# Kernel optimization log

Hardware: AMD Instinct MI355X
Metric: run time of the kernel (lower is better)

## Reference

```python
import jax, jax.numpy as jnp
import numpy as np

STRIDE = 16      # image -> feature stride (224 -> 14)
POOL = 7         # ROI pool output grid
FG_HI = 0.85
FG_LO = 0.5


def setup_inputs() -> dict:
    key = jax.random.key(0)
    ks = jax.random.split(key, 8)
    B, N, M, K = 4, 128, 16, 80
    Cf, Tf, Cs, Ts, H, W = 256, 32, 2048, 8, 14, 14
    fast = jax.random.normal(ks[0], (B, Cf, Tf, H, W), jnp.float32)
    slow = jax.random.normal(ks[1], (B, Cs, Ts, H, W), jnp.float32)
    # valid gt boxes inside 224x224
    xy = jax.random.uniform(ks[2], (B, M, 2)) * 160.0
    wh = 32.0 + jax.random.uniform(ks[3], (B, M, 2)) * 48.0
    gt = jnp.concatenate([xy, xy + wh], axis=-1)
    # proposals: first M coincide with gt (guarantees IoU>=0.85 foreground), rest random
    pxy = jax.random.uniform(ks[4], (B, N - M, 2)) * 160.0
    pwh = 16.0 + jax.random.uniform(ks[5], (B, N - M, 2)) * 64.0
    props = jnp.concatenate([gt, jnp.concatenate([pxy, pxy + pwh], axis=-1)], axis=1)
    gt_classes = (jax.random.uniform(ks[6], (B, M, K)) < 0.1).astype(jnp.float32)
    C = Cf + Cs
    W_cls = jax.random.normal(ks[7], (C, K), jnp.float32) * 0.02
    b_cls = jnp.zeros((K,), jnp.float32)
    return dict(fast_feature=fast, slow_feature=slow, proposal_bboxes=props,
                gt_bboxes_batch=gt, gt_classes_batch=gt_classes,
                W_cls=W_cls, b_cls=b_cls)


def _iou(a, b):
    # a: [B,N,4], b: [B,M,4] (x1,y1,x2,y2) -> [B,N,M]
    tl = jnp.maximum(a[:, :, None, :2], b[:, None, :, :2])
    br = jnp.minimum(a[:, :, None, 2:], b[:, None, :, 2:])
    inter = jnp.prod(jnp.clip(br - tl, 0.0), axis=-1)
    area_a = jnp.prod(a[:, :, 2:] - a[:, :, :2], axis=-1)[:, :, None]
    area_b = jnp.prod(b[:, :, 2:] - b[:, :, :2], axis=-1)[:, None, :]
    return inter / (area_a + area_b - inter)


def _roi_pool(feat, boxes):
    # feat: [B,C,H,W]; boxes: [B,N,4] in image coords -> [B,N,P,P,C]
    B, C, H, W = feat.shape
    fb = boxes / STRIDE
    x1, y1, x2, y2 = fb[..., 0], fb[..., 1], fb[..., 2], fb[..., 3]
    grid = (jnp.arange(POOL, dtype=feat.dtype) + 0.5) / POOL          # [P]
    cy = y1[..., None] + grid * (y2 - y1)[..., None]                  # [B,N,P]
    cx = x1[..., None] + grid * (x2 - x1)[..., None]                  # [B,N,P]
    iy = jnp.clip(jnp.floor(cy), 0, H - 1).astype(jnp.int32)
    ix = jnp.clip(jnp.floor(cx), 0, W - 1).astype(jnp.int32)
    ft = jnp.transpose(feat, (0, 2, 3, 1))                            # [B,H,W,C]
    bidx = jnp.arange(B)[:, None, None, None]
    return ft[bidx, iy[:, :, :, None], ix[:, :, None, :]]             # [B,N,P,P,C]


def reference(fast_feature, slow_feature, proposal_bboxes, gt_bboxes_batch,
              gt_classes_batch, W_cls, b_cls):
    # temporal average pooling (AvgPool3d over full T) + channel concat, fast first
    fast = fast_feature.mean(axis=2)
    slow = slow_feature.mean(axis=2)
    feature = jnp.concatenate([fast, slow], axis=1)                   # [B,C,H,W]

    # IoU-based foreground assignment
    ious = _iou(proposal_bboxes, gt_bboxes_batch)                     # [B,N,M]
    max_ious = ious.max(axis=2)                                       # [B,N]
    assign = ious.argmax(axis=2)                                      # [B,N]
    fg_hi = max_ious >= FG_HI
    fg = jnp.where(fg_hi.any(), fg_hi, max_ious >= FG_LO)             # global fallback
    labels = jnp.take_along_axis(gt_classes_batch, assign[:, :, None], axis=1)  # [B,N,K]

    # ROI pooling (dense over all proposals; non-fg are masked out of the loss)
    pool = _roi_pool(feature, proposal_bboxes)                        # [B,N,P,P,C]
    hid = pool.mean(axis=(2, 3))                                      # [B,N,C]
    logits = jnp.einsum('bnc,ck->bnk', hid, W_cls) + b_cls            # [B,N,K]

    # multilabel soft margin loss per proposal (mean over classes)
    per = -(labels * jax.nn.log_sigmoid(logits)
            + (1.0 - labels) * jax.nn.log_sigmoid(-logits)).mean(axis=-1)  # [B,N]
    fgf = fg.astype(per.dtype)
    cnt = fgf.sum(axis=1)
    cross_entropies = jnp.where(cnt > 0, (per * fgf).sum(axis=1) / jnp.maximum(cnt, 1.0), 0.0)
    return cross_entropies  # [B]
```

## Files before the change

kernel.cpp:

```cpp
#include <hip/hip_runtime.h>
#include <math.h>

#define BB 4
#define NN 128
#define MM 16
#define KK 80
#define CF 256
#define CSL 2048
#define CT 2304
#define TFAST 32
#define TSLOW 8
#define HH 14
#define WW 14
#define HWQ 196
#define NQ4 49

#define G_OFF      0
#define G_SIZE     (BB*HWQ*KK)
#define FGF_OFF    (G_OFF + G_SIZE)
#define ASSIGN_OFF (FGF_OFF + BB*NN)
#define NUM_OFF    (ASSIGN_OFF + BB*NN)
#define CNT_OFF    (NUM_OFF + BB)
#define CTR_OFF    (CNT_OFF + BB)
#define P_OFF      (CTR_OFF + 8)

#define NSPLIT 64
#define MAXCH  43
#define P_SIZE (NSPLIT*G_SIZE)

__global__ __launch_bounds__(256) void k12_fused(const float* __restrict__ fastp,
                                                 const float* __restrict__ slowp,
                                                 const float* __restrict__ Wc,
                                                 float* __restrict__ ws,
                                                 int use_partials) {
    __shared__ float sfeat[MAXCH*HWQ + 64];
    __shared__ float sW[MAXCH*KK];
    int bid = blockIdx.x;
    int b = bid >> 6;
    int r = bid & 63;
    int gc0, nch, T, isfast;
    if (r < 16) { isfast = 1; gc0 = r * 16; nch = 16; T = TFAST; }
    else {
        int s = r - 16;
        int c0s = (s < 32) ? (43 * s) : (1376 + 42 * (s - 32));
        nch = (s < 32) ? 43 : 42;
        gc0 = CF + c0s; T = TSLOW; isfast = 0;
    }
    int tid = threadIdx.x;

    const float4* base = isfast
        ? ((const float4*)fastp + (size_t)(b * CF + gc0) * TFAST * NQ4)
        : ((const float4*)slowp + (size_t)(b * CSL + (gc0 - CF)) * TSLOW * NQ4);
    const float scale = 1.f / (float)T;
    int ntasks = nch * NQ4;
    for (int x = tid; x < ntasks; x += 256) {
        int cl = x / NQ4;
        int q  = x - cl * NQ4;
        const float4* p = base + (size_t)cl * T * NQ4 + q;
        float4 a = make_float4(0.f, 0.f, 0.f, 0.f);
        #pragma unroll 8
        for (int t = 0; t < T; ++t) {
            float4 v = p[t * NQ4];
            a.x += v.x; a.y += v.y; a.z += v.z; a.w += v.w;
        }
        a.x *= scale; a.y *= scale; a.z *= scale; a.w *= scale;
        ((float4*)sfeat)[cl * NQ4 + q] = a;
    }
    const float4* wsrc = (const float4*)Wc + (size_t)gc0 * (KK / 4);
    int wtasks = nch * (KK / 4);
    for (int x = tid; x < wtasks; x += 256) ((float4*)sW)[x] = wsrc[x];
    __syncthreads();

    int cg = tid & 31;
    int kq = tid >> 5;
    float acc[7][10];
    #pragma unroll
    for (int j = 0; j < 7; ++j)
        #pragma unroll
        for (int i = 0; i < 10; ++i) acc[j][i] = 0.f;

    const float* fr = sfeat + cg;
    const float* wr = sW + kq * 10;
    for (int c = 0; c < nch; ++c) {
        float w[10];
        #pragma unroll
        for (int i = 0; i < 10; ++i) w[i] = wr[c * KK + i];
        #pragma unroll
        for (int j = 0; j < 7; ++j) {
            float fv = fr[c * HWQ + 32 * j];
            #pragma unroll
            for (int i = 0; i < 10; ++i) acc[j][i] += fv * w[i];
        }
    }

    int k0 = kq * 10;
    if (use_partials) {
        float* P = ws + P_OFF + (size_t)r * G_SIZE + (size_t)b * (KK * HWQ);
        #pragma unroll
        for (int j = 0; j < 7; ++j) {
            int cell = cg + 32 * j;
            if (cell < HWQ) {
                #pragma unroll
                for (int i = 0; i < 10; ++i) P[(k0 + i) * HWQ + cell] = acc[j][i];
            }
        }
    } else {
        float* g = ws + G_OFF + (size_t)b * HWQ * KK;
        #pragma unroll
        for (int j = 0; j < 7; ++j) {
            int cell = cg + 32 * j;
            if (cell < HWQ) {
                #pragma unroll
                for (int i = 0; i < 10; ++i) atomicAdd(&g[cell * KK + k0 + i], acc[j][i]);
            }
        }
    }
}

__global__ __launch_bounds__(256) void kz_zero(float* __restrict__ ws) {
    int idx = blockIdx.x * 256 + threadIdx.x;
    if (idx < G_SIZE) ws[G_OFF + idx] = 0.f;
}

#define RED_BLOCKS ((G_SIZE + 511) / 512)
__global__ __launch_bounds__(512) void k2b_assign(const float* __restrict__ props,
                                                  const float* __restrict__ gtb,
                                                  float* __restrict__ ws,
                                                  int use_partials) {
    int blk = blockIdx.x;
    int t = threadIdx.x;
    if (blk < RED_BLOCKS) {
        if (!use_partials) return;
        int ridx = blk * 512 + t;
        if (ridx < G_SIZE) {
            const float* P = ws + P_OFF;
            float s = 0.f;
            #pragma unroll 16
            for (int cs = 0; cs < NSPLIT; ++cs) s += P[(size_t)cs * G_SIZE + ridx];
            int b    = ridx / (KK * HWQ);
            int rem  = ridx - b * (KK * HWQ);
            int k    = rem / HWQ;
            int cell = rem - k * HWQ;
            ws[G_OFF + (size_t)b * HWQ * KK + cell * KK + k] = s;
        }
        return;
    }
    __shared__ float sgt[BB*MM*4];
    __shared__ float sfg[BB*NN];
    __shared__ int sany;
    if (t < BB*MM*4) sgt[t] = gtb[t];
    if (t == 0) sany = 0;
    __syncthreads();
    int b = t >> 7;
    float x1 = props[t*4+0], y1 = props[t*4+1], x2 = props[t*4+2], y2 = props[t*4+3];
    float aa = (x2 - x1) * (y2 - y1);
    float best = -1.f; int arg = 0;
    for (int m = 0; m < MM; ++m) {
        const float* g = &sgt[(b*MM + m)*4];
        float tlx = fmaxf(x1, g[0]), tly = fmaxf(y1, g[1]);
        float brx = fminf(x2, g[2]), bry = fminf(y2, g[3]);
        float inter = fmaxf(brx - tlx, 0.f) * fmaxf(bry - tly, 0.f);
        float ab = (g[2] - g[0]) * (g[3] - g[1]);
        float iou = inter / (aa + ab - inter);
        if (iou > best) { best = iou; arg = m; }
    }
    if (best >= 0.85f) atomicOr(&sany, 1);
    __syncthreads();
    float fg = sany ? (best >= 0.85f ? 1.f : 0.f) : (best >= 0.5f ? 1.f : 0.f);
    sfg[t] = fg;
    ws[FGF_OFF + t] = fg;
    ((int*)ws)[ASSIGN_OFF + t] = arg;
    __syncthreads();
    if (t < BB) {
        float s = 0.f;
        for (int i = 0; i < NN; ++i) s += sfg[t*NN + i];
        ws[CNT_OFF + t] = s;
        ws[NUM_OFF + t] = 0.f;
    }
    if (t == 0) ((int*)ws)[CTR_OFF] = 0;
}

__device__ __forceinline__ float logsig(float x) {
    return fminf(x, 0.f) - log1pf(expf(-fabsf(x)));
}

__global__ __launch_bounds__(128) void k3b_loss(const float* __restrict__ props,
                                                const float* __restrict__ gtc,
                                                const float* __restrict__ bcls,
                                                float* __restrict__ ws,
                                                float* __restrict__ out) {
    int p = blockIdx.x;
    int b = p >> 7;
    int t = threadIdx.x;
    __shared__ int cells[49];
    __shared__ float red[128];
    if (ws[FGF_OFF + p] != 0.f) {
        if (t < 49) {
            int gy = t / 7, gx = t % 7;
            float x1 = props[p*4+0] * (1.f/16.f);
            float y1 = props[p*4+1] * (1.f/16.f);
            float x2 = props[p*4+2] * (1.f/16.f);
            float y2 = props[p*4+3] * (1.f/16.f);
            float gry = ((float)gy + 0.5f) / 7.f;
            float grx = ((float)gx + 0.5f) / 7.f;
            float cy = y1 + gry * (y2 - y1);
            float cx = x1 + grx * (x2 - x1);
            int iy = (int)floorf(cy); iy = min(max(iy, 0), HH-1);
            int ix = (int)floorf(cx); ix = min(max(ix, 0), WW-1);
            cells[t] = iy * WW + ix;
        }
        __syncthreads();
        float lk = 0.f;
        if (t < KK) {
            float acc = 0.f;
            const float* Gb = ws + G_OFF + b * HWQ * KK + t;
            #pragma unroll 7
            for (int g = 0; g < 49; ++g) acc += Gb[cells[g] * KK];
            float logit = acc * (1.f/49.f) + bcls[t];
            int a = ((const int*)ws)[ASSIGN_OFF + p];
            float y = gtc[(b*MM + a)*KK + t];
            lk = -(y * logsig(logit) + (1.f - y) * logsig(-logit));
        }
        red[t] = lk;
        __syncthreads();
        for (int s = 64; s > 0; s >>= 1) {
            if (t < s) red[t] += red[t + s];
            __syncthreads();
        }
        if (t == 0) atomicAdd(&ws[NUM_OFF + b], red[0] * (1.f/KK));
    }
    if (t == 0) {
        __threadfence();
        int old = atomicAdd(&((int*)ws)[CTR_OFF], 1);
        if (old == BB*NN - 1) {
            __threadfence();
            #pragma unroll
            for (int bb = 0; bb < BB; ++bb) {
                float num = atomicAdd(&ws[NUM_OFF + bb], 0.f);
                float c = ws[CNT_OFF + bb];
                out[bb] = (c > 0.f) ? num / c : 0.f;
            }
        }
    }
}

extern "C" void kernel_launch(void* const* d_in, const int* in_sizes, int n_in,
                              void* d_out, int out_size, void* d_ws, size_t ws_size,
                              hipStream_t stream) {
    const float* fastp = (const float*)d_in[0];
    const float* slowp = (const float*)d_in[1];
    const float* props = (const float*)d_in[2];
    const float* gtb   = (const float*)d_in[3];
    const float* gtc   = (const float*)d_in[4];
    const float* Wc    = (const float*)d_in[5];
    const float* bcls  = (const float*)d_in[6];
    float* ws  = (float*)d_ws;
    float* out = (float*)d_out;

    const size_t need = (size_t)(P_OFF + P_SIZE) * sizeof(float);
    const int use_partials = (ws_size >= need) ? 1 : 0;

    if (!use_partials)
        kz_zero<<<(G_SIZE + 255)/256, 256, 0, stream>>>(ws);
    k12_fused<<<BB * NSPLIT, 256, 0, stream>>>(fastp, slowp, Wc, ws, use_partials);
    k2b_assign<<<RED_BLOCKS + 1, 512, 0, stream>>>(props, gtb, ws, use_partials);
    k3b_loss<<<BB*NN, 128, 0, stream>>>(props, gtc, bcls, ws, out);
}
```

Before: 137.5 us.

## Split temporal mean into separate wide kernel before per-chunk GEMM

Takes the temporal averaging of the fast and slow features out of the 256-block fused kernel and puts it in its own kernel, launched with one thread per float4 per channel. That kernel writes a time-averaged feature map to workspace. A second kernel then loads that map into shared memory and runs the channel-by-class partial GEMM. The goal is to spread the bandwidth-bound read of about 150MB across many more threads than 256 blocks can keep busy. The cost is an extra launch and a write and re-read of the ~7MB mean map, and the workspace must now be large enough to hold it, otherwise the atomic fallback path runs.

```diff
diff --git a/kernel.cpp b/kernel.cpp
--- a/kernel.cpp
+++ b/kernel.cpp
@@ -22,17 +22,116 @@
 #define NUM_OFF    (ASSIGN_OFF + BB*NN)
 #define CNT_OFF    (NUM_OFF + BB)
 #define CTR_OFF    (CNT_OFF + BB)
-#define P_OFF      (CTR_OFF + 8)
+#define FM_OFF     (CTR_OFF + 8)
+#define FM_SIZE    (BB*CT*HWQ)
+#define P_OFF      (FM_OFF + FM_SIZE)
 
 #define NSPLIT 64
 #define MAXCH  43
 #define P_SIZE (NSPLIT*G_SIZE)
 
+#define MTASKS (BB*CT*NQ4)
+
+__global__ __launch_bounds__(256) void kmean(const float* __restrict__ fastp,
+                                             const float* __restrict__ slowp,
+                                             float* __restrict__ ws) {
+    int idx = blockIdx.x * 256 + threadIdx.x;
+    if (idx >= MTASKS) return;
+    int bc = idx / NQ4;
+    int q  = idx - bc * NQ4;
+    int b  = bc / CT;
+    int c  = bc - b * CT;
+    float4 a = make_float4(0.f, 0.f, 0.f, 0.f);
+    if (c < CF) {
+        const float4* p = (const float4*)fastp + (size_t)(b * CF + c) * TFAST * NQ4 + q;
+        #pragma unroll 8
+        for (int t = 0; t < TFAST; ++t) {
+            float4 v = p[t * NQ4];
+            a.x += v.x; a.y += v.y; a.z += v.z; a.w += v.w;
+        }
+        const float s = 1.f / (float)TFAST;
+        a.x *= s; a.y *= s; a.z *= s; a.w *= s;
+    } else {
+        const float4* p = (const float4*)slowp + (size_t)(b * CSL + (c - CF)) * TSLOW * NQ4 + q;
+        #pragma unroll
+        for (int t = 0; t < TSLOW; ++t) {
+            float4 v = p[t * NQ4];
+            a.x += v.x; a.y += v.y; a.z += v.z; a.w += v.w;
+        }
+        const float s = 1.f / (float)TSLOW;
+        a.x *= s; a.y *= s; a.z *= s; a.w *= s;
+    }
+    ((float4*)(ws + FM_OFF))[(size_t)bc * NQ4 + q] = a;
+}
+
+__global__ __launch_bounds__(256) void kgemm(const float* __restrict__ Wc,
+                                             float* __restrict__ ws) {
+    __shared__ float sfeat[MAXCH*HWQ + 64];
+    __shared__ float sW[MAXCH*KK];
+    int bid = blockIdx.x;
+    int b = bid >> 6;
+    int r = bid & 63;
+    int gc0, nch;
+    if (r < 16) { gc0 = r * 16; nch = 16; }
+    else {
+        int s = r - 16;
+        int c0s = (s < 32) ? (43 * s) : (1376 + 42 * (s - 32));
+        nch = (s < 32) ? 43 : 42;
+        gc0 = CF + c0s;
+    }
+    int tid = threadIdx.x;
+
+    const float4* fsrc = (const float4*)(ws + FM_OFF) + (size_t)(b * CT + gc0) * NQ4;
+    int ntasks = nch * NQ4;
+    for (int x = tid; x < ntasks; x += 256) ((float4*)sfeat)[x] = fsrc[x];
+    const float4* wsrc = (const float4*)Wc + (size_t)gc0 * (KK / 4);
+    int wtasks = nch * (KK / 4);
+    for (int x = tid; x < wtasks; x += 256) ((float4*)sW)[x] = wsrc[x];
+    __syncthreads();
+
+    int cg = tid & 31;
+    int kq = tid >> 5;
+    float acc[7][10];
+    #pragma unroll
+    for (int j = 0; j < 7; ++j)
+        #pragma unroll
+        for (int i = 0; i < 10; ++i) acc[j][i] = 0.f;
+
+    const float* fr = sfeat + cg;
+    const float* wr = sW + kq * 10;
+    for (int c = 0; c < nch; ++c) {
+        float w[10];
+        #pragma unroll
+        for (int i = 0; i < 10; ++i) w[i] = wr[c * KK + i];
+        #pragma unroll
+        for (int j = 0; j < 7; ++j) {
+            float fv = fr[c * HWQ + 32 * j];
+            #pragma unroll
+            for (int i = 0; i < 10; ++i) acc[j][i] += fv * w[i];
+        }
+    }
+
+    int k0 = kq * 10;
+    float* P = ws + P_OFF + (size_t)r * G_SIZE + (size_t)b * (KK * HWQ);
+    #pragma unroll
+    for (int j = 0; j < 7; ++j) {
+        int cell = cg + 32 * j;
+        if (cell < HWQ) {
+            #pragma unroll
+            for (int i = 0; i < 10; ++i) P[(k0 + i) * HWQ + cell] = acc[j][i];
+        }
+    }
+}
+
+__global__ __launch_bounds__(256) void kz_zero(float* __restrict__ ws) {
+    int idx = blockIdx.x * 256 + threadIdx.x;
+    if (idx < G_SIZE) ws[G_OFF + idx] = 0.f;
+}
+
 __global__ __launch_bounds__(256) void k12_fused(const float* __restrict__ fastp,
                                                  const float* __restrict__ slowp,
                                                  const float* __restrict__ Wc,
-                                                 float* __restrict__ ws,
-                                                 int use_partials) {
+                                                 float* __restrict__ ws) {
     __shared__ float sfeat[MAXCH*HWQ + 64];
     __shared__ float sW[MAXCH*KK];
     int bid = blockIdx.x;
@@ -94,32 +193,15 @@
     }
 
     int k0 = kq * 10;
-    if (use_partials) {
-        float* P = ws + P_OFF + (size_t)r * G_SIZE + (size_t)b * (KK * HWQ);
-        #pragma unroll
-        for (int j = 0; j < 7; ++j) {
-            int cell = cg + 32 * j;
-            if (cell < HWQ) {
-                #pragma unroll
-                for (int i = 0; i < 10; ++i) P[(k0 + i) * HWQ + cell] = acc[j][i];
-            }
-        }
-    } else {
-        float* g = ws + G_OFF + (size_t)b * HWQ * KK;
-        #pragma unroll
-        for (int j = 0; j < 7; ++j) {
-            int cell = cg + 32 * j;
-            if (cell < HWQ) {
-                #pragma unroll
-                for (int i = 0; i < 10; ++i) atomicAdd(&g[cell * KK + k0 + i], acc[j][i]);
-            }
-        }
-    }
-}
-
-__global__ __launch_bounds__(256) void kz_zero(float* __restrict__ ws) {
-    int idx = blockIdx.x * 256 + threadIdx.x;
-    if (idx < G_SIZE) ws[G_OFF + idx] = 0.f;
+    float* g = ws + G_OFF + (size_t)b * HWQ * KK;
+    #pragma unroll
+    for (int j = 0; j < 7; ++j) {
+        int cell = cg + 32 * j;
+        if (cell < HWQ) {
+            #pragma unroll
+            for (int i = 0; i < 10; ++i) atomicAdd(&g[cell * KK + k0 + i], acc[j][i]);
+        }
+    }
 }
 
 #define RED_BLOCKS ((G_SIZE + 511) / 512)
@@ -260,9 +342,13 @@
     const size_t need = (size_t)(P_OFF + P_SIZE) * sizeof(float);
     const int use_partials = (ws_size >= need) ? 1 : 0;
 
-    if (!use_partials)
+    if (use_partials) {
+        kmean<<<(MTASKS + 255)/256, 256, 0, stream>>>(fastp, slowp, ws);
+        kgemm<<<BB * NSPLIT, 256, 0, stream>>>(Wc, ws);
+    } else {
         kz_zero<<<(G_SIZE + 255)/256, 256, 0, stream>>>(ws);
-    k12_fused<<<BB * NSPLIT, 256, 0, stream>>>(fastp, slowp, Wc, ws, use_partials);
+        k12_fused<<<BB * NSPLIT, 256, 0, stream>>>(fastp, slowp, Wc, ws);
+    }
     k2b_assign<<<RED_BLOCKS + 1, 512, 0, stream>>>(props, gtb, ws, use_partials);
     k3b_loss<<<BB*NN, 128, 0, stream>>>(props, gtc, bcls, ws, out);
 }
```

New measurement: 140.5 us. 1.02x slower.

## Fuse all stages into one cooperative kernel with grid-wide syncs

Applied to the files above, without the earlier changes.

Merges the channel-reduction GEMV, partial-sum reduction, IoU assignment, and loss stages into a single cooperative kernel of 256 blocks, separated by grid.sync barriers. This removes three separate kernel launches and the gaps between them. Each block now handles two proposals in the loss phase. The risks are grid-sync overhead, the requirement that all blocks be co-resident, and the shared-memory union limiting occupancy. If the cooperative launch fails, the code falls back to the atomic path.

```diff
diff --git a/kernel.cpp b/kernel.cpp
--- a/kernel.cpp
+++ b/kernel.cpp
@@ -1,5 +1,8 @@
 #include <hip/hip_runtime.h>
+#include <hip/hip_cooperative_groups.h>
 #include <math.h>
+
+namespace cg = cooperative_groups;
 
 #define BB 4
 #define NN 128
@@ -28,11 +31,223 @@
 #define MAXCH  43
 #define P_SIZE (NSPLIT*G_SIZE)
 
+#define GRID 256
+#define RB   245
+
+__device__ __forceinline__ float logsig(float x) {
+    return fminf(x, 0.f) - log1pf(expf(-fabsf(x)));
+}
+
+__global__ __launch_bounds__(256) void kall(const float* __restrict__ fastp,
+                                            const float* __restrict__ slowp,
+                                            const float* __restrict__ props,
+                                            const float* __restrict__ gtb,
+                                            const float* __restrict__ gtc,
+                                            const float* __restrict__ Wc,
+                                            const float* __restrict__ bcls,
+                                            float* __restrict__ ws,
+                                            float* __restrict__ out) {
+    cg::grid_group grid = cg::this_grid();
+    __shared__ union alignas(16) {
+        struct { float sfeat[MAXCH*HWQ + 64]; float sW[MAXCH*KK]; } a;
+        struct { float sgt[BB*MM*4]; float sfg[BB*NN]; int sany; } b;
+        struct { int cells[2][49]; float red[2][128]; } c;
+    } sm;
+
+    const int bid = blockIdx.x;
+    const int tid = threadIdx.x;
+
+    {
+        int b = bid >> 6;
+        int r = bid & 63;
+        int gc0, nch, T, isfast;
+        if (r < 16) { isfast = 1; gc0 = r * 16; nch = 16; T = TFAST; }
+        else {
+            int s = r - 16;
+            int c0s = (s < 32) ? (43 * s) : (1376 + 42 * (s - 32));
+            nch = (s < 32) ? 43 : 42;
+            gc0 = CF + c0s; T = TSLOW; isfast = 0;
+        }
+
+        const float4* base = isfast
+            ? ((const float4*)fastp + (size_t)(b * CF + gc0) * TFAST * NQ4)
+            : ((const float4*)slowp + (size_t)(b * CSL + (gc0 - CF)) * TSLOW * NQ4);
+        const float scale = 1.f / (float)T;
+        int ntasks = nch * NQ4;
+        for (int x = tid; x < ntasks; x += 256) {
+            int cl = x / NQ4;
+            int q  = x - cl * NQ4;
+            const float4* p = base + (size_t)cl * T * NQ4 + q;
+            float4 a = make_float4(0.f, 0.f, 0.f, 0.f);
+            #pragma unroll 8
+            for (int t = 0; t < T; ++t) {
+                float4 v = p[t * NQ4];
+                a.x += v.x; a.y += v.y; a.z += v.z; a.w += v.w;
+            }
+            a.x *= scale; a.y *= scale; a.z *= scale; a.w *= scale;
+            ((float4*)sm.a.sfeat)[cl * NQ4 + q] = a;
+        }
+        const float4* wsrc = (const float4*)Wc + (size_t)gc0 * (KK / 4);
+        int wtasks = nch * (KK / 4);
+        for (int x = tid; x < wtasks; x += 256) ((float4*)sm.a.sW)[x] = wsrc[x];
+        __syncthreads();
+
+        int cg_ = tid & 31;
+        int kq  = tid >> 5;
+        float acc[7][10];
+        #pragma unroll
+        for (int j = 0; j < 7; ++j)
+            #pragma unroll
+            for (int i = 0; i < 10; ++i) acc[j][i] = 0.f;
+
+        const float* fr = sm.a.sfeat + cg_;
+        const float* wr = sm.a.sW + kq * 10;
+        for (int c = 0; c < nch; ++c) {
+            float w[10];
+            #pragma unroll
+            for (int i = 0; i < 10; ++i) w[i] = wr[c * KK + i];
+            #pragma unroll
+            for (int j = 0; j < 7; ++j) {
+                float fv = fr[c * HWQ + 32 * j];
+                #pragma unroll
+                for (int i = 0; i < 10; ++i) acc[j][i] += fv * w[i];
+            }
+        }
+
+        int k0 = kq * 10;
+        float* P = ws + P_OFF + (size_t)r * G_SIZE + (size_t)b * (KK * HWQ);
+        #pragma unroll
+        for (int j = 0; j < 7; ++j) {
+            int cell = cg_ + 32 * j;
+            if (cell < HWQ) {
+                #pragma unroll
+                for (int i = 0; i < 10; ++i) P[(k0 + i) * HWQ + cell] = acc[j][i];
+            }
+        }
+    }
+
+    __threadfence();
+    grid.sync();
+
+    if (bid < RB) {
+        int ridx = bid * 256 + tid;
+        const float* P = ws + P_OFF;
+        float s = 0.f;
+        #pragma unroll 16
+        for (int cs = 0; cs < NSPLIT; ++cs) s += P[(size_t)cs * G_SIZE + ridx];
+        int b    = ridx / (KK * HWQ);
+        int rem  = ridx - b * (KK * HWQ);
+        int k    = rem / HWQ;
+        int cell = rem - k * HWQ;
+        ws[G_OFF + (size_t)b * HWQ * KK + cell * KK + k] = s;
+    } else if (bid == GRID - 1) {
+        if (tid < BB*MM*4) sm.b.sgt[tid] = gtb[tid];
+        if (tid == 0) sm.b.sany = 0;
+        __syncthreads();
+        float bestv[2]; int argv[2]; int flag = 0;
+        #pragma unroll
+        for (int h = 0; h < 2; ++h) {
+            int p = tid + 256 * h;
+            int b = p >> 7;
+            float x1 = props[p*4+0], y1 = props[p*4+1], x2 = props[p*4+2], y2 = props[p*4+3];
+            float aa = (x2 - x1) * (y2 - y1);
+            float best = -1.f; int arg = 0;
+            for (int m = 0; m < MM; ++m) {
+                const float* g = &sm.b.sgt[(b*MM + m)*4];
+                float tlx = fmaxf(x1, g[0]), tly = fmaxf(y1, g[1]);
+                float brx = fminf(x2, g[2]), bry = fminf(y2, g[3]);
+                float inter = fmaxf(brx - tlx, 0.f) * fmaxf(bry - tly, 0.f);
+                float ab = (g[2] - g[0]) * (g[3] - g[1]);
+                float iou = inter / (aa + ab - inter);
+                if (iou > best) { best = iou; arg = m; }
+            }
+            bestv[h] = best; argv[h] = arg;
+            if (best >= 0.85f) flag = 1;
+        }
+        if (flag) atomicOr(&sm.b.sany, 1);
+        __syncthreads();
+        int any = sm.b.sany;
+        #pragma unroll
+        for (int h = 0; h < 2; ++h) {
+            int p = tid + 256 * h;
+            float fg = any ? (bestv[h] >= 0.85f ? 1.f : 0.f) : (bestv[h] >= 0.5f ? 1.f : 0.f);
+            sm.b.sfg[p] = fg;
+            ws[FGF_OFF + p] = fg;
+            ((int*)ws)[ASSIGN_OFF + p] = argv[h];
+        }
+        __syncthreads();
+        if (tid < BB) {
+            float s = 0.f;
+            for (int i = 0; i < NN; ++i) s += sm.b.sfg[tid*NN + i];
+            ws[CNT_OFF + tid] = s;
+            ws[NUM_OFF + tid] = 0.f;
+        }
+    }
+
+    __threadfence();
+    grid.sync();
+
+    {
+        int h = tid >> 7;
+        int t = tid & 127;
+        int p = (bid << 1) | h;
+        int b = p >> 7;
+        float fgf = ws[FGF_OFF + p];
+        if (t < 49) {
+            int gy = t / 7, gx = t % 7;
+            float x1 = props[p*4+0] * (1.f/16.f);
+            float y1 = props[p*4+1] * (1.f/16.f);
+            float x2 = props[p*4+2] * (1.f/16.f);
+            float y2 = props[p*4+3] * (1.f/16.f);
+            float gry = ((float)gy + 0.5f) / 7.f;
+            float grx = ((float)gx + 0.5f) / 7.f;
+            float cy = y1 + gry * (y2 - y1);
+            float cx = x1 + grx * (x2 - x1);
+            int iy = (int)floorf(cy); iy = min(max(iy, 0), HH-1);
+            int ix = (int)floorf(cx); ix = min(max(ix, 0), WW-1);
+            sm.c.cells[h][t] = iy * WW + ix;
+        }
+        __syncthreads();
+        float lk = 0.f;
+        if (t < KK) {
+            float acc = 0.f;
+            const float* Gb = ws + G_OFF + b * HWQ * KK + t;
+            #pragma unroll 7
+            for (int g = 0; g < 49; ++g) acc += Gb[sm.c.cells[h][g] * KK];
+            float logit = acc * (1.f/49.f) + bcls[t];
+            int a = ((const int*)ws)[ASSIGN_OFF + p];
+            float y = gtc[(b*MM + a)*KK + t];
+            lk = -(y * logsig(logit) + (1.f - y) * logsig(-logit));
+        }
+        sm.c.red[h][t] = lk;
+        __syncthreads();
+        for (int s = 64; s > 0; s >>= 1) {
+            if (t < s) sm.c.red[h][t] += sm.c.red[h][t + s];
+            __syncthreads();
+        }
+        if (t == 0 && fgf != 0.f)
+            atomicAdd(&ws[NUM_OFF + b], sm.c.red[h][0] * (1.f/KK));
+    }
+
+    __threadfence();
+    grid.sync();
+
+    if (bid == 0 && tid < BB) {
+        float num = ws[NUM_OFF + tid];
+        float c   = ws[CNT_OFF + tid];
+        out[tid] = (c > 0.f) ? num / c : 0.f;
+    }
+}
+
+__global__ __launch_bounds__(256) void kz_zero(float* __restrict__ ws) {
+    int idx = blockIdx.x * 256 + threadIdx.x;
+    if (idx < G_SIZE) ws[G_OFF + idx] = 0.f;
+}
+
 __global__ __launch_bounds__(256) void k12_fused(const float* __restrict__ fastp,
                                                  const float* __restrict__ slowp,
                                                  const float* __restrict__ Wc,
-                                                 float* __restrict__ ws,
-                                                 int use_partials) {
+                                                 float* __restrict__ ws) {
     __shared__ float sfeat[MAXCH*HWQ + 64];
     __shared__ float sW[MAXCH*KK];
     int bid = blockIdx.x;
@@ -71,7 +286,7 @@
     for (int x = tid; x < wtasks; x += 256) ((float4*)sW)[x] = wsrc[x];
     __syncthreads();
 
-    int cg = tid & 31;
+    int cg_ = tid & 31;
     int kq = tid >> 5;
     float acc[7][10];
     #pragma unroll
@@ -79,7 +294,7 @@
         #pragma unroll
         for (int i = 0; i < 10; ++i) acc[j][i] = 0.f;
 
-    const float* fr = sfeat + cg;
+    const float* fr = sfeat + cg_;
     const float* wr = sW + kq * 10;
     for (int c = 0; c < nch; ++c) {
         float w[10];
@@ -94,32 +309,15 @@
     }
 
     int k0 = kq * 10;
-    if (use_partials) {
-        float* P = ws + P_OFF + (size_t)r * G_SIZE + (size_t)b * (KK * HWQ);
-        #pragma unroll
-        for (int j = 0; j < 7; ++j) {
-            int cell = cg + 32 * j;
-            if (cell < HWQ) {
-                #pragma unroll
-                for (int i = 0; i < 10; ++i) P[(k0 + i) * HWQ + cell] = acc[j][i];
-            }
-        }
-    } else {
-        float* g = ws + G_OFF + (size_t)b * HWQ * KK;
-        #pragma unroll
-        for (int j = 0; j < 7; ++j) {
-            int cell = cg + 32 * j;
-            if (cell < HWQ) {
-                #pragma unroll
-                for (int i = 0; i < 10; ++i) atomicAdd(&g[cell * KK + k0 + i], acc[j][i]);
-            }
-        }
-    }
-}
-
-__global__ __launch_bounds__(256) void kz_zero(float* __restrict__ ws) {
-    int idx = blockIdx.x * 256 + threadIdx.x;
-    if (idx < G_SIZE) ws[G_OFF + idx] = 0.f;
+    float* g = ws + G_OFF + (size_t)b * HWQ * KK;
+    #pragma unroll
+    for (int j = 0; j < 7; ++j) {
+        int cell = cg_ + 32 * j;
+        if (cell < HWQ) {
+            #pragma unroll
+            for (int i = 0; i < 10; ++i) atomicAdd(&g[cell * KK + k0 + i], acc[j][i]);
+        }
+    }
 }
 
 #define RED_BLOCKS ((G_SIZE + 511) / 512)
@@ -178,10 +376,6 @@
         ws[NUM_OFF + t] = 0.f;
     }
     if (t == 0) ((int*)ws)[CTR_OFF] = 0;
-}
-
-__device__ __forceinline__ float logsig(float x) {
-    return fminf(x, 0.f) - log1pf(expf(-fabsf(x)));
 }
 
 __global__ __launch_bounds__(128) void k3b_loss(const float* __restrict__ props,
@@ -258,11 +452,17 @@
     float* out = (float*)d_out;
 
     const size_t need = (size_t)(P_OFF + P_SIZE) * sizeof(float);
-    const int use_partials = (ws_size >= need) ? 1 : 0;
-
-    if (!use_partials)
-        kz_zero<<<(G_SIZE + 255)/256, 256, 0, stream>>>(ws);
-    k12_fused<<<BB * NSPLIT, 256, 0, stream>>>(fastp, slowp, Wc, ws, use_partials);
-    k2b_assign<<<RED_BLOCKS + 1, 512, 0, stream>>>(props, gtb, ws, use_partials);
+    if (ws_size >= need) {
+        void* args[] = {(void*)&fastp, (void*)&slowp, (void*)&props, (void*)&gtb,
+                        (void*)&gtc, (void*)&Wc, (void*)&bcls, (void*)&ws, (void*)&out};
+        hipError_t e = hipLaunchCooperativeKernel(reinterpret_cast<void*>(kall),
+                                                  dim3(GRID), dim3(256), args, 0, stream);
+        if (e == hipSuccess) return;
+        (void)hipGetLastError();
+    }
+
+    kz_zero<<<(G_SIZE + 255)/256, 256, 0, stream>>>(ws);
+    k12_fused<<<BB * NSPLIT, 256, 0, stream>>>(fastp, slowp, Wc, ws);
+    k2b_assign<<<RED_BLOCKS + 1, 512, 0, stream>>>(props, gtb, ws, 0);
     k3b_loss<<<BB*NN, 128, 0, stream>>>(props, gtc, bcls, ws, out);
 }
```

Result: slower. 324.3 us (+135.8%).
